# Kernel tuning notes

Measured on AMD Instinct MI355X. Metric: run time of the kernel, lower is better.

## Reference

```python
import jax, jax.numpy as jnp
import numpy as np

N_LAYERS = 3
N_USERS = 100000
N_ITEMS = 50000
N_NODES = N_USERS + N_ITEMS
EMBED_DIM = 64
NNZ = 8000000


def setup_inputs() -> dict:
    key = jax.random.key(0)
    k1, k2, k3, k4, k5 = jax.random.split(key, 5)
    # Xavier-uniform-like init scale (gain=1): sqrt(6/(fan_in+fan_out))
    bound_u = float(np.sqrt(6.0 / (N_USERS + EMBED_DIM)))
    bound_i = float(np.sqrt(6.0 / (N_ITEMS + EMBED_DIM)))
    user_embedding = jax.random.uniform(k1, (N_USERS, EMBED_DIM), jnp.float32, -bound_u, bound_u)
    item_embedding = jax.random.uniform(k2, (N_ITEMS, EMBED_DIM), jnp.float32, -bound_i, bound_i)
    adj_rows = jax.random.randint(k3, (NNZ,), 0, N_NODES, jnp.int32)
    adj_cols = jax.random.randint(k4, (NNZ,), 0, N_NODES, jnp.int32)
    # normalized adjacency values (positive, small)
    adj_vals = jax.random.uniform(k5, (NNZ,), jnp.float32) * 0.02
    return {
        "user_embedding": user_embedding,
        "item_embedding": item_embedding,
        "adj_rows": adj_rows,
        "adj_cols": adj_cols,
        "adj_vals": adj_vals,
    }


def spmm(rows, cols, vals, x):
    # y[r] = sum_{(r,c) in nnz} vals * x[c]   (COO SpMM via gather + segment_sum)
    gathered = x[cols] * vals[:, None]            # [nnz, D]
    return jax.ops.segment_sum(gathered, rows, num_segments=N_NODES)


def reference(user_embedding, item_embedding, adj_rows, adj_cols, adj_vals):
    emb = jnp.concatenate([user_embedding, item_embedding], axis=0)  # [N, D]
    acc = emb
    for _ in range(N_LAYERS):
        emb = spmm(adj_rows, adj_cols, adj_vals, emb)
        acc = acc + emb
    final = acc / (N_LAYERS + 1)
    return final[:N_USERS], final[N_USERS:]
```

## Files before the change

kernel.cpp:

```cpp
#include <hip/hip_runtime.h>

#define N_USERS 100000
#define N_ITEMS 50000
#define N_NODES 150000
#define EMBED_DIM 64

#define BUCKET_SHIFT 9
#define BUCKET_ROWS 512
#define NB 293
#define NBLK 2048

__device__ inline float4 bf4_to_f4(ushort4 u) {
    float4 f;
    f.x = __uint_as_float((unsigned)u.x << 16);
    f.y = __uint_as_float((unsigned)u.y << 16);
    f.z = __uint_as_float((unsigned)u.z << 16);
    f.w = __uint_as_float((unsigned)u.w << 16);
    return f;
}

__device__ inline unsigned short f_to_bf(float f) {
    unsigned u = __float_as_uint(f);
    return (unsigned short)((u + 0x7FFFu + ((u >> 16) & 1u)) >> 16);
}

__global__ void init_kernel(const float4* __restrict__ user,
                            const float4* __restrict__ item,
                            ushort4* __restrict__ xbf,
                            float4* __restrict__ acc,
                            int n_user4, int total4) {
    int i = blockIdx.x * blockDim.x + threadIdx.x;
    if (i < total4) {
        float4 v = (i < n_user4) ? user[i] : item[i - n_user4];
        acc[i] = v;
        ushort4 b;
        b.x = f_to_bf(v.x); b.y = f_to_bf(v.y);
        b.z = f_to_bf(v.z); b.w = f_to_bf(v.w);
        xbf[i] = b;
    }
}

__global__ __launch_bounds__(256) void part_count_kernel(const int* __restrict__ rows,
                                                         int* __restrict__ blk_cnt, int nnz) {
    __shared__ int cnt[NB];
    for (int i = threadIdx.x; i < NB; i += 256) cnt[i] = 0;
    __syncthreads();
    int b = blockIdx.x;
    int chunk = (nnz + NBLK - 1) / NBLK;
    int s = b * chunk, e = min(nnz, s + chunk);
    for (int i = s + threadIdx.x; i < e; i += 256)
        atomicAdd(&cnt[rows[i] >> BUCKET_SHIFT], 1);
    __syncthreads();
    for (int i = threadIdx.x; i < NB; i += 256) blk_cnt[b * NB + i] = cnt[i];
}

__global__ __launch_bounds__(256) void scan_blocks_kernel(int* __restrict__ blk_cnt,
                                                          int* __restrict__ bkt_tot) {
    __shared__ int psum[256];
    int nb = blockIdx.x, tid = threadIdx.x;
    int v[8]; int s = 0;
#pragma unroll
    for (int j = 0; j < 8; ++j) {
        v[j] = blk_cnt[(8 * tid + j) * NB + nb];
        s += v[j];
    }
    psum[tid] = s; __syncthreads();
    for (int off = 1; off < 256; off <<= 1) {
        int t = (tid >= off) ? psum[tid - off] : 0;
        __syncthreads();
        psum[tid] += t;
        __syncthreads();
    }
    int run = psum[tid] - s;
#pragma unroll
    for (int j = 0; j < 8; ++j) {
        blk_cnt[(8 * tid + j) * NB + nb] = run;
        run += v[j];
    }
    if (tid == 255) bkt_tot[nb] = psum[255];
}

__global__ __launch_bounds__(256) void scan_buckets_kernel(const int* __restrict__ bkt_tot,
                                                           int* __restrict__ bucket_start, int nnz) {
    __shared__ int lds[256];
    int tid = threadIdx.x;
    int v[2]; int s = 0;
#pragma unroll
    for (int j = 0; j < 2; ++j) {
        int idx = tid * 2 + j;
        v[j] = (idx < NB) ? bkt_tot[idx] : 0;
        s += v[j];
    }
    lds[tid] = s; __syncthreads();
    for (int off = 1; off < 256; off <<= 1) {
        int t = (tid >= off) ? lds[tid - off] : 0;
        __syncthreads();
        lds[tid] += t;
        __syncthreads();
    }
    int run = lds[tid] - s;
#pragma unroll
    for (int j = 0; j < 2; ++j) {
        int idx = tid * 2 + j;
        if (idx < NB) bucket_start[idx] = run;
        run += v[j];
    }
    if (tid == 0) bucket_start[NB] = nnz;
}

__global__ __launch_bounds__(256) void partition_kernel(const int* __restrict__ rows,
                                                        const int* __restrict__ cols,
                                                        const float* __restrict__ vals,
                                                        const int* __restrict__ blk_cnt,
                                                        const int* __restrict__ bucket_start,
                                                        int2* __restrict__ part, int nnz) {
    __shared__ int cur[NB];
    int b = blockIdx.x;
    for (int i = threadIdx.x; i < NB; i += 256)
        cur[i] = bucket_start[i] + blk_cnt[b * NB + i];
    __syncthreads();
    int chunk = (nnz + NBLK - 1) / NBLK;
    int s = b * chunk, e = min(nnz, s + chunk);
    for (int i = s + threadIdx.x; i < e; i += 256) {
        int r = rows[i];
        int nb = r >> BUCKET_SHIFT;
        int rl = r & (BUCKET_ROWS - 1);
        int pos = atomicAdd(&cur[nb], 1);
        part[pos] = make_int2((rl << 18) | cols[i], __float_as_int(vals[i]));
    }
}

__global__ __launch_bounds__(256) void bucket_sort_kernel(const int2* __restrict__ part,
                                                          const int* __restrict__ bucket_start,
                                                          int* __restrict__ row_ptr,
                                                          int2* __restrict__ edges, int nnz) {
    __shared__ int cnt[BUCKET_ROWS];
    __shared__ int off[BUCKET_ROWS];
    __shared__ int psum[256];
    int nb = blockIdx.x, tid = threadIdx.x;
    int base = bucket_start[nb];
    int cntE = bucket_start[nb + 1] - base;

    cnt[tid] = 0; cnt[tid + 256] = 0;
    __syncthreads();
    for (int i = tid; i < cntE; i += 256)
        atomicAdd(&cnt[part[base + i].x >> 18], 1);
    __syncthreads();

    int c0 = cnt[2 * tid], c1 = cnt[2 * tid + 1];
    int s = c0 + c1;
    psum[tid] = s; __syncthreads();
    for (int o = 1; o < 256; o <<= 1) {
        int t = (tid >= o) ? psum[tid - o] : 0;
        __syncthreads();
        psum[tid] += t;
        __syncthreads();
    }
    int excl = psum[tid] - s;
    off[2 * tid] = excl;
    off[2 * tid + 1] = excl + c0;

    int r0 = nb << BUCKET_SHIFT;
    int ra = r0 + 2 * tid, rb = r0 + 2 * tid + 1;
    if (ra < N_NODES) row_ptr[ra] = base + excl;
    if (rb < N_NODES) row_ptr[rb] = base + excl + c0;
    __syncthreads();

    for (int i = tid; i < cntE; i += 256) {
        int2 ev = part[base + i];
        int rl = ev.x >> 18;
        int rank = atomicAdd(&off[rl], 1);
        edges[base + rank] = make_int2(ev.x & 0x3FFFF, ev.y);
    }
    if (nb == 0 && tid == 0) row_ptr[N_NODES] = nnz;
}

__global__ __launch_bounds__(256) void spmm_csr_kernel(
        const int* __restrict__ row_ptr, const int2* __restrict__ edges,
        const ushort4* __restrict__ xbf,
        ushort4* __restrict__ ybf, float4* __restrict__ out4,
        float final_scale, int write_y) {
    int wid = (blockIdx.x * blockDim.x + threadIdx.x) >> 6;
    int lane = threadIdx.x & 63;
    if (wid >= N_NODES) return;

    int start = row_ptr[wid];
    int nj = row_ptr[wid + 1] - start;
    int g  = lane >> 4;
    int gl = lane & 15;

    const int2* ep = edges + start;
    float4 acc0 = make_float4(0.f, 0.f, 0.f, 0.f);
    float4 acc1 = make_float4(0.f, 0.f, 0.f, 0.f);

    int jmax = (nj + 7) >> 3;
    for (int j = 0; j < jmax; ++j) {
        int i0 = (j << 3) + g;
        int i1 = i0 + 4;
        bool ok0 = i0 < nj;
        bool ok1 = i1 < nj;
        int2 ev0 = ep[ok0 ? i0 : 0];
        int2 ev1 = ep[ok1 ? i1 : 0];
        float v0 = ok0 ? __int_as_float(ev0.y) : 0.0f;
        float v1 = ok1 ? __int_as_float(ev1.y) : 0.0f;
        float4 xv0 = bf4_to_f4(xbf[ev0.x * 16 + gl]);
        float4 xv1 = bf4_to_f4(xbf[ev1.x * 16 + gl]);
        acc0.x += v0 * xv0.x;  acc0.y += v0 * xv0.y;
        acc0.z += v0 * xv0.z;  acc0.w += v0 * xv0.w;
        acc1.x += v1 * xv1.x;  acc1.y += v1 * xv1.y;
        acc1.z += v1 * xv1.z;  acc1.w += v1 * xv1.w;
    }

    float4 acc;
    acc.x = acc0.x + acc1.x;
    acc.y = acc0.y + acc1.y;
    acc.z = acc0.z + acc1.z;
    acc.w = acc0.w + acc1.w;

#pragma unroll
    for (int off = 16; off < 64; off <<= 1) {
        acc.x += __shfl_xor(acc.x, off, 64);
        acc.y += __shfl_xor(acc.y, off, 64);
        acc.z += __shfl_xor(acc.z, off, 64);
        acc.w += __shfl_xor(acc.w, off, 64);
    }

    if (lane < 16) {
        int o = wid * 16 + gl;
        if (write_y) {
            ushort4 b;
            b.x = f_to_bf(acc.x); b.y = f_to_bf(acc.y);
            b.z = f_to_bf(acc.z); b.w = f_to_bf(acc.w);
            ybf[o] = b;
        }
        float4 ov = out4[o];
        ov.x = (ov.x + acc.x) * final_scale;
        ov.y = (ov.y + acc.y) * final_scale;
        ov.z = (ov.z + acc.z) * final_scale;
        ov.w = (ov.w + acc.w) * final_scale;
        out4[o] = ov;
    }
}

extern "C" void kernel_launch(void* const* d_in, const int* in_sizes, int n_in,
                              void* d_out, int out_size, void* d_ws, size_t ws_size,
                              hipStream_t stream) {
    const float* user = (const float*)d_in[0];
    const float* item = (const float*)d_in[1];
    const int*   rows = (const int*)d_in[2];
    const int*   cols = (const int*)d_in[3];
    const float* vals = (const float*)d_in[4];
    float* out = (float*)d_out;

    const int nnz = in_sizes[2];
    const size_t nfloats = (size_t)N_NODES * EMBED_DIM;
    const int total4 = (int)(nfloats / 4);
    const int n_user4 = (N_USERS * EMBED_DIM) / 4;

    char* ws = (char*)d_ws;
    size_t off = 0;
    auto alloc = [&](size_t bytes) { size_t p = off; off += (bytes + 255) & ~(size_t)255; return p; };
    size_t o_part   = alloc(((size_t)nnz + 8) * sizeof(int2));
    size_t o_rptr   = alloc((N_NODES + 1) * sizeof(int));
    size_t o_blkcnt = alloc((size_t)NBLK * NB * sizeof(int));
    size_t o_btot   = alloc((NB + 1) * sizeof(int));
    size_t o_bstart = alloc((NB + 1) * sizeof(int));
    size_t o_edges  = alloc(((size_t)nnz + 8) * sizeof(int2));

    int2* part    = (int2*)(ws + o_part);
    int* row_ptr  = (int*)(ws + o_rptr);
    int* blk_cnt  = (int*)(ws + o_blkcnt);
    int* bkt_tot  = (int*)(ws + o_btot);
    int* bstart   = (int*)(ws + o_bstart);
    int2* edges   = (int2*)(ws + o_edges);
    ushort4* xbf  = (ushort4*)(ws + o_part);
    ushort4* ybf  = (ushort4*)(ws + o_part + (size_t)N_NODES * EMBED_DIM * 2);
    (void)ws_size;

    part_count_kernel<<<NBLK, 256, 0, stream>>>(rows, blk_cnt, nnz);
    scan_blocks_kernel<<<NB, 256, 0, stream>>>(blk_cnt, bkt_tot);
    scan_buckets_kernel<<<1, 256, 0, stream>>>(bkt_tot, bstart, nnz);
    partition_kernel<<<NBLK, 256, 0, stream>>>(rows, cols, vals, blk_cnt, bstart, part, nnz);
    bucket_sort_kernel<<<NB, 256, 0, stream>>>(part, bstart, row_ptr, edges, nnz);

    int iblocks = (total4 + 255) / 256;
    init_kernel<<<iblocks, 256, 0, stream>>>((const float4*)user, (const float4*)item,
                                             xbf, (float4*)out, n_user4, total4);

    ushort4* x = xbf; ushort4* y = ybf;
    int sblocks = (N_NODES * 64 + 255) / 256;
    for (int layer = 0; layer < 3; ++layer) {
        float fs = (layer == 2) ? 0.25f : 1.0f;
        int wy = (layer == 2) ? 0 : 1;
        spmm_csr_kernel<<<sblocks, 256, 0, stream>>>(row_ptr, edges,
                                                     (const ushort4*)x,
                                                     y, (float4*)out, fs, wy);
        ushort4* t = x; x = y; y = t;
    }
}
```

Baseline: 882.0 us.

## Pre-sort edges by column bin and widen SpMM gathers to 16-byte loads

Adds a column-bin pass inside each row bucket so that edges within a row are loosely ordered by source column, which should improve cache locality of the embedding gathers. The bucket sort moves to 1024-thread blocks and reads the column-binned edges. The SpMM kernel now has 8 lanes per row, each loading 16 bytes (8 bf16 values), so each wave processes 8 edges per step instead of 4. The cost is an extra preprocessing kernel with an extra pass over all edges, plus more registers and more shuffle-reduction steps in the SpMM kernel.

```diff
diff --git a/kernel.cpp b/kernel.cpp
--- a/kernel.cpp
+++ b/kernel.cpp
@@ -9,20 +9,14 @@
 #define BUCKET_ROWS 512
 #define NB 293
 #define NBLK 2048
-
-__device__ inline float4 bf4_to_f4(ushort4 u) {
-    float4 f;
-    f.x = __uint_as_float((unsigned)u.x << 16);
-    f.y = __uint_as_float((unsigned)u.y << 16);
-    f.z = __uint_as_float((unsigned)u.z << 16);
-    f.w = __uint_as_float((unsigned)u.w << 16);
-    return f;
-}
+#define NBIN 10
 
 __device__ inline unsigned short f_to_bf(float f) {
     unsigned u = __float_as_uint(f);
     return (unsigned short)((u + 0x7FFFu + ((u >> 16) & 1u)) >> 16);
 }
+__device__ inline float bf_lo(int w) { return __uint_as_float((unsigned)w << 16); }
+__device__ inline float bf_hi(int w) { return __uint_as_float((unsigned)w & 0xFFFF0000u); }
 
 __global__ void init_kernel(const float4* __restrict__ user,
                             const float4* __restrict__ item,
@@ -130,10 +124,61 @@
     }
 }
 
-__global__ __launch_bounds__(256) void bucket_sort_kernel(const int2* __restrict__ part,
-                                                          const int* __restrict__ bucket_start,
-                                                          int* __restrict__ row_ptr,
-                                                          int2* __restrict__ edges, int nnz) {
+__global__ __launch_bounds__(1024) void colbin_sort_kernel(const int2* __restrict__ part,
+                                                           const int* __restrict__ bucket_start,
+                                                           int2* __restrict__ csorted) {
+    __shared__ int cnt[NBIN];
+    __shared__ int off[NBIN];
+    int nb = blockIdx.x, tid = threadIdx.x;
+    int lane = tid & 63;
+    int base = bucket_start[nb];
+    int cntE = bucket_start[nb + 1] - base;
+
+    if (tid < NBIN) cnt[tid] = 0;
+    __syncthreads();
+
+    for (int i = tid; i < cntE; i += 1024) {
+        int bin = (part[base + i].x & 0x3FFFF) >> 14;
+#pragma unroll
+        for (int b = 0; b < NBIN; ++b) {
+            unsigned long long m = __ballot(bin == b);
+            if (bin == b) {
+                int pre = __popcll(m & ((1ull << lane) - 1ull));
+                if (pre == 0) atomicAdd(&cnt[b], __popcll(m));
+            }
+        }
+    }
+    __syncthreads();
+    if (tid == 0) {
+        int run = 0;
+        for (int b = 0; b < NBIN; ++b) { off[b] = run; run += cnt[b]; }
+    }
+    __syncthreads();
+
+    for (int i = tid; i < cntE; i += 1024) {
+        int2 ev = part[base + i];
+        int bin = (ev.x & 0x3FFFF) >> 14;
+        int pos = 0;
+#pragma unroll
+        for (int b = 0; b < NBIN; ++b) {
+            unsigned long long m = __ballot(bin == b);
+            if (bin == b) {
+                int pre = __popcll(m & ((1ull << lane) - 1ull));
+                int ldr = __ffsll((unsigned long long)m) - 1;
+                int bp = 0;
+                if (pre == 0) bp = atomicAdd(&off[b], __popcll(m));
+                bp = __shfl(bp, ldr, 64);
+                pos = bp + pre;
+            }
+        }
+        csorted[base + pos] = ev;
+    }
+}
+
+__global__ __launch_bounds__(1024) void bucket_sort_kernel(const int2* __restrict__ csorted,
+                                                           const int* __restrict__ bucket_start,
+                                                           int* __restrict__ row_ptr,
+                                                           int2* __restrict__ edges, int nnz) {
     __shared__ int cnt[BUCKET_ROWS];
     __shared__ int off[BUCKET_ROWS];
     __shared__ int psum[256];
@@ -141,33 +186,39 @@
     int base = bucket_start[nb];
     int cntE = bucket_start[nb + 1] - base;
 
-    cnt[tid] = 0; cnt[tid + 256] = 0;
-    __syncthreads();
-    for (int i = tid; i < cntE; i += 256)
-        atomicAdd(&cnt[part[base + i].x >> 18], 1);
-    __syncthreads();
-
-    int c0 = cnt[2 * tid], c1 = cnt[2 * tid + 1];
-    int s = c0 + c1;
-    psum[tid] = s; __syncthreads();
+    if (tid < BUCKET_ROWS) cnt[tid] = 0;
+    __syncthreads();
+    for (int i = tid; i < cntE; i += 1024)
+        atomicAdd(&cnt[csorted[base + i].x >> 18], 1);
+    __syncthreads();
+
+    int c0 = 0, c1 = 0, s = 0;
+    if (tid < 256) {
+        c0 = cnt[2 * tid]; c1 = cnt[2 * tid + 1];
+        s = c0 + c1;
+        psum[tid] = s;
+    }
+    __syncthreads();
     for (int o = 1; o < 256; o <<= 1) {
-        int t = (tid >= o) ? psum[tid - o] : 0;
-        __syncthreads();
-        psum[tid] += t;
-        __syncthreads();
-    }
-    int excl = psum[tid] - s;
-    off[2 * tid] = excl;
-    off[2 * tid + 1] = excl + c0;
-
-    int r0 = nb << BUCKET_SHIFT;
-    int ra = r0 + 2 * tid, rb = r0 + 2 * tid + 1;
-    if (ra < N_NODES) row_ptr[ra] = base + excl;
-    if (rb < N_NODES) row_ptr[rb] = base + excl + c0;
-    __syncthreads();
-
-    for (int i = tid; i < cntE; i += 256) {
-        int2 ev = part[base + i];
+        int t = 0;
+        if (tid < 256 && tid >= o) t = psum[tid - o];
+        __syncthreads();
+        if (tid < 256) psum[tid] += t;
+        __syncthreads();
+    }
+    if (tid < 256) {
+        int excl = psum[tid] - s;
+        off[2 * tid] = excl;
+        off[2 * tid + 1] = excl + c0;
+        int r0 = nb << BUCKET_SHIFT;
+        int ra = r0 + 2 * tid, rb = ra + 1;
+        if (ra < N_NODES) row_ptr[ra] = base + excl;
+        if (rb < N_NODES) row_ptr[rb] = base + excl + c0;
+    }
+    __syncthreads();
+
+    for (int i = tid; i < cntE; i += 1024) {
+        int2 ev = csorted[base + i];
         int rl = ev.x >> 18;
         int rank = atomicAdd(&off[rl], 1);
         edges[base + rank] = make_int2(ev.x & 0x3FFFF, ev.y);
@@ -177,7 +228,7 @@
 
 __global__ __launch_bounds__(256) void spmm_csr_kernel(
         const int* __restrict__ row_ptr, const int2* __restrict__ edges,
-        const ushort4* __restrict__ xbf,
+        const int4* __restrict__ x16,
         ushort4* __restrict__ ybf, float4* __restrict__ out4,
         float final_scale, int write_y) {
     int wid = (blockIdx.x * blockDim.x + threadIdx.x) >> 6;
@@ -186,59 +237,67 @@
 
     int start = row_ptr[wid];
     int nj = row_ptr[wid + 1] - start;
-    int g  = lane >> 4;
-    int gl = lane & 15;
+    int g  = lane >> 3;
+    int gl = lane & 7;
 
     const int2* ep = edges + start;
-    float4 acc0 = make_float4(0.f, 0.f, 0.f, 0.f);
-    float4 acc1 = make_float4(0.f, 0.f, 0.f, 0.f);
-
-    int jmax = (nj + 7) >> 3;
+    float a0[8] = {0,0,0,0,0,0,0,0};
+    float a1[8] = {0,0,0,0,0,0,0,0};
+
+    int jmax = (nj + 15) >> 4;
     for (int j = 0; j < jmax; ++j) {
-        int i0 = (j << 3) + g;
-        int i1 = i0 + 4;
+        int i0 = (j << 4) + g;
+        int i1 = i0 + 8;
         bool ok0 = i0 < nj;
         bool ok1 = i1 < nj;
-        int2 ev0 = ep[ok0 ? i0 : 0];
-        int2 ev1 = ep[ok1 ? i1 : 0];
-        float v0 = ok0 ? __int_as_float(ev0.y) : 0.0f;
-        float v1 = ok1 ? __int_as_float(ev1.y) : 0.0f;
-        float4 xv0 = bf4_to_f4(xbf[ev0.x * 16 + gl]);
-        float4 xv1 = bf4_to_f4(xbf[ev1.x * 16 + gl]);
-        acc0.x += v0 * xv0.x;  acc0.y += v0 * xv0.y;
-        acc0.z += v0 * xv0.z;  acc0.w += v0 * xv0.w;
-        acc1.x += v1 * xv1.x;  acc1.y += v1 * xv1.y;
-        acc1.z += v1 * xv1.z;  acc1.w += v1 * xv1.w;
-    }
-
-    float4 acc;
-    acc.x = acc0.x + acc1.x;
-    acc.y = acc0.y + acc1.y;
-    acc.z = acc0.z + acc1.z;
-    acc.w = acc0.w + acc1.w;
-
-#pragma unroll
-    for (int off = 16; off < 64; off <<= 1) {
-        acc.x += __shfl_xor(acc.x, off, 64);
-        acc.y += __shfl_xor(acc.y, off, 64);
-        acc.z += __shfl_xor(acc.z, off, 64);
-        acc.w += __shfl_xor(acc.w, off, 64);
-    }
-
-    if (lane < 16) {
-        int o = wid * 16 + gl;
+        int2 e0 = ep[ok0 ? i0 : 0];
+        int2 e1 = ep[ok1 ? i1 : 0];
+        float v0 = ok0 ? __int_as_float(e0.y) : 0.0f;
+        float v1 = ok1 ? __int_as_float(e1.y) : 0.0f;
+        int4 q0 = x16[e0.x * 8 + gl];
+        int4 q1 = x16[e1.x * 8 + gl];
+        a0[0] += v0 * bf_lo(q0.x);  a0[1] += v0 * bf_hi(q0.x);
+        a0[2] += v0 * bf_lo(q0.y);  a0[3] += v0 * bf_hi(q0.y);
+        a0[4] += v0 * bf_lo(q0.z);  a0[5] += v0 * bf_hi(q0.z);
+        a0[6] += v0 * bf_lo(q0.w);  a0[7] += v0 * bf_hi(q0.w);
+        a1[0] += v1 * bf_lo(q1.x);  a1[1] += v1 * bf_hi(q1.x);
+        a1[2] += v1 * bf_lo(q1.y);  a1[3] += v1 * bf_hi(q1.y);
+        a1[4] += v1 * bf_lo(q1.z);  a1[5] += v1 * bf_hi(q1.z);
+        a1[6] += v1 * bf_lo(q1.w);  a1[7] += v1 * bf_hi(q1.w);
+    }
+
+    float a[8];
+#pragma unroll
+    for (int k = 0; k < 8; ++k) a[k] = a0[k] + a1[k];
+
+#pragma unroll
+    for (int off = 8; off < 64; off <<= 1) {
+#pragma unroll
+        for (int k = 0; k < 8; ++k) a[k] += __shfl_xor(a[k], off, 64);
+    }
+
+    if (lane < 8) {
+        int o = wid * 16 + gl * 2;
         if (write_y) {
-            ushort4 b;
-            b.x = f_to_bf(acc.x); b.y = f_to_bf(acc.y);
-            b.z = f_to_bf(acc.z); b.w = f_to_bf(acc.w);
-            ybf[o] = b;
+            ushort4 b0, b1;
+            b0.x = f_to_bf(a[0]); b0.y = f_to_bf(a[1]);
+            b0.z = f_to_bf(a[2]); b0.w = f_to_bf(a[3]);
+            b1.x = f_to_bf(a[4]); b1.y = f_to_bf(a[5]);
+            b1.z = f_to_bf(a[6]); b1.w = f_to_bf(a[7]);
+            ybf[o] = b0; ybf[o + 1] = b1;
         }
         float4 ov = out4[o];
-        ov.x = (ov.x + acc.x) * final_scale;
-        ov.y = (ov.y + acc.y) * final_scale;
-        ov.z = (ov.z + acc.z) * final_scale;
-        ov.w = (ov.w + acc.w) * final_scale;
+        ov.x = (ov.x + a[0]) * final_scale;
+        ov.y = (ov.y + a[1]) * final_scale;
+        ov.z = (ov.z + a[2]) * final_scale;
+        ov.w = (ov.w + a[3]) * final_scale;
         out4[o] = ov;
+        float4 ow = out4[o + 1];
+        ow.x = (ow.x + a[4]) * final_scale;
+        ow.y = (ow.y + a[5]) * final_scale;
+        ow.z = (ow.z + a[6]) * final_scale;
+        ow.w = (ow.w + a[7]) * final_scale;
+        out4[o + 1] = ow;
     }
 }
 
@@ -265,23 +324,25 @@
     size_t o_blkcnt = alloc((size_t)NBLK * NB * sizeof(int));
     size_t o_btot   = alloc((NB + 1) * sizeof(int));
     size_t o_bstart = alloc((NB + 1) * sizeof(int));
-    size_t o_edges  = alloc(((size_t)nnz + 8) * sizeof(int2));
+    size_t o_csort  = alloc(((size_t)nnz + 8) * sizeof(int2));
 
     int2* part    = (int2*)(ws + o_part);
     int* row_ptr  = (int*)(ws + o_rptr);
     int* blk_cnt  = (int*)(ws + o_blkcnt);
     int* bkt_tot  = (int*)(ws + o_btot);
     int* bstart   = (int*)(ws + o_bstart);
-    int2* edges   = (int2*)(ws + o_edges);
-    ushort4* xbf  = (ushort4*)(ws + o_part);
-    ushort4* ybf  = (ushort4*)(ws + o_part + (size_t)N_NODES * EMBED_DIM * 2);
+    int2* csorted = (int2*)(ws + o_csort);
+    int2* edges   = part;
+    ushort4* xbf  = (ushort4*)(ws + o_csort);
+    ushort4* ybf  = (ushort4*)(ws + o_csort + (size_t)N_NODES * EMBED_DIM * 2);
     (void)ws_size;
 
     part_count_kernel<<<NBLK, 256, 0, stream>>>(rows, blk_cnt, nnz);
     scan_blocks_kernel<<<NB, 256, 0, stream>>>(blk_cnt, bkt_tot);
     scan_buckets_kernel<<<1, 256, 0, stream>>>(bkt_tot, bstart, nnz);
     partition_kernel<<<NBLK, 256, 0, stream>>>(rows, cols, vals, blk_cnt, bstart, part, nnz);
-    bucket_sort_kernel<<<NB, 256, 0, stream>>>(part, bstart, row_ptr, edges, nnz);
+    colbin_sort_kernel<<<NB, 1024, 0, stream>>>(part, bstart, csorted);
+    bucket_sort_kernel<<<NB, 1024, 0, stream>>>(csorted, bstart, row_ptr, edges, nnz);
 
     int iblocks = (total4 + 255) / 256;
     init_kernel<<<iblocks, 256, 0, stream>>>((const float4*)user, (const float4*)item,
@@ -293,7 +354,7 @@
         float fs = (layer == 2) ? 0.25f : 1.0f;
         int wy = (layer == 2) ? 0 : 1;
         spmm_csr_kernel<<<sblocks, 256, 0, stream>>>(row_ptr, edges,
-                                                     (const ushort4*)x,
+                                                     (const int4*)x,
                                                      y, (float4*)out, fs, wy);
         ushort4* t = x; x = y; y = t;
     }
```

Measured after the change: 919.5 us. 1.04x slower.
